# Kernel tuning notes

Hardware: AMD Instinct MI355X
Metric: run time of the kernel (lower is better)

Reference implementation:

```python
import jax, jax.numpy as jnp
import numpy as np

B, S, D, H, FC, O = 256, 512, 512, 512, 64, 2
E_CONST = 2.7183  # constant used in map_elapse_time


def setup_inputs() -> dict:
    key = jax.random.key(0)
    ks = jax.random.split(key, 24)
    std = 0.1
    w = lambda k, a, b: jax.random.normal(k, (a, b), jnp.float32) * std
    return {
        "x": jax.random.normal(ks[0], (B, S, D), jnp.float32),
        "time": jax.random.uniform(ks[1], (B, S), jnp.float32) * 10.0,  # positive elapsed times
        "Wi": w(ks[2], D, H), "Ui": w(ks[3], H, H), "bi": jnp.ones((H,), jnp.float32),
        "Wf": w(ks[4], D, H), "Uf": w(ks[5], H, H), "bf": jnp.ones((H,), jnp.float32),
        "Wog": w(ks[6], D, H), "Uog": w(ks[7], H, H), "bog": jnp.ones((H,), jnp.float32),
        "Wc": w(ks[8], D, H), "Uc": w(ks[9], H, H), "bc": jnp.ones((H,), jnp.float32),
        "W_decomp": w(ks[10], H, H), "b_decomp": jnp.ones((H,), jnp.float32),
        "Wo": w(ks[11], H, FC), "bo": jnp.ones((FC,), jnp.float32),
        "W_softmax": w(ks[12], FC, O), "b_softmax": jnp.ones((O,), jnp.float32),
    }


def reference(x, time, Wi, Ui, bi, Wf, Uf, bf, Wog, Uog, bog, Wc, Uc, bc,
              W_decomp, b_decomp, Wo, bo, W_softmax, b_softmax):
    Bsz, _, _ = x.shape
    Hd = Ui.shape[0]
    xs = jnp.swapaxes(x, 0, 1)                     # [S, B, D]
    ts = jnp.swapaxes(time, 0, 1)[..., None]       # [S, B, 1]
    h0 = jnp.zeros((Bsz, Hd), x.dtype)

    def step(carry, inp):
        h, c = carry
        x_t, t_t = inp
        # time-decay cell decomposition
        T = 1.0 / jnp.log(t_t + E_CONST)           # [B, 1] broadcast over H
        C_ST = jnp.tanh(c @ W_decomp + b_decomp)
        c = c - C_ST + T * C_ST
        # gates
        i = jax.nn.sigmoid(x_t @ Wi + h @ Ui + bi)
        f = jax.nn.sigmoid(x_t @ Wf + h @ Uf + bf)
        o = jax.nn.sigmoid(x_t @ Wog + h @ Uog + bog)
        Cn = jnp.tanh(x_t @ Wc + h @ Uc + bc)
        c = f * c + i * Cn
        h = o * jnp.tanh(c)
        return (h, c), None

    (h_last, _), _ = jax.lax.scan(step, (h0, h0), (xs, ts))
    # output head on last hidden state (dropout omitted: inference reference)
    fc = jax.nn.relu(h_last @ Wo + bo)
    return fc @ W_softmax + b_softmax             # [B, output_dim]
```

## Files before the change

### kernel.cpp

```cpp
#include <hip/hip_runtime.h>


typedef _Float16 f16;
typedef _Float16 f16x8 __attribute__((ext_vector_type(8)));
typedef float f32x4 __attribute__((ext_vector_type(4)));

#define B_ 256
#define S_ 512
#define D_ 512
#define H_ 512

#define WS_WTG  0u
#define WS_WTD  4194304u
#define WS_H16  4718592u
#define WS_C16  5242880u
#define WS_HF32 5767168u
#define WS_BAR  6291456u
#define WS_END  6295552u

__device__ __forceinline__ float fast_sigmoid(float x) {
  return 1.0f / (1.0f + __expf(-x));
}
__device__ __forceinline__ float fast_tanh(float x) {
  x = fminf(15.0f, fmaxf(-15.0f, x));
  float e = __expf(2.0f * x);
  return (e - 1.0f) / (e + 1.0f);
}
__device__ __forceinline__ unsigned pack_f16x2(float a, float b) {
  union { f16 h[2]; unsigned u; } p;
  p.h[0] = (f16)a; p.h[1] = (f16)b;
  return p.u;
}
__device__ __forceinline__ unsigned ld_agent(const unsigned* p) {
  return __hip_atomic_load(p, __ATOMIC_RELAXED, __HIP_MEMORY_SCOPE_AGENT);
}
__device__ __forceinline__ void st_agent(unsigned* p, unsigned v) {
  __hip_atomic_store(p, v, __ATOMIC_RELAXED, __HIP_MEMORY_SCOPE_AGENT);
}

__global__ void pack_weights(const float* __restrict__ Wi, const float* __restrict__ Ui,
                             const float* __restrict__ Wf, const float* __restrict__ Uf,
                             const float* __restrict__ Wog, const float* __restrict__ Uog,
                             const float* __restrict__ Wc, const float* __restrict__ Uc,
                             const float* __restrict__ Wd,
                             f16* __restrict__ wtg, f16* __restrict__ wtd)
{
  const int idx = blockIdx.x * 256 + threadIdx.x;
  if (idx < 2048 * 1024) {
    const int n = idx >> 10, k = idx & 1023;
    const int g = n >> 9, j = n & 511;
    const float* W[8] = {Wi, Ui, Wf, Uf, Wog, Uog, Wc, Uc};
    const float* src = W[(g << 1) + (k >> 9)];
    wtg[idx] = (f16)src[(size_t)(k & 511) * 512 + j];
  } else {
    const int i2 = idx - 2048 * 1024;
    const int n = i2 >> 9, k = i2 & 511;
    wtd[i2] = (f16)Wd[(size_t)k * 512 + n];
  }
}

__global__ void __launch_bounds__(256, 1)
tlstm_main(const float* __restrict__ x, const float* __restrict__ tim,
           const float* __restrict__ bi, const float* __restrict__ bf,
           const float* __restrict__ bog, const float* __restrict__ bc,
           const float* __restrict__ bdec,
           const f16* __restrict__ wtg, const f16* __restrict__ wtd,
           f16* __restrict__ h16, f16* __restrict__ c16,
           float* __restrict__ hf32, int* __restrict__ bar)
{
  __shared__ __align__(16) f16 Ag[16][1032];
  __shared__ __align__(16) f16 Ad[16][520];
  __shared__ float accS[10][272];
  __shared__ float biasS[10][16];

  const int tid  = threadIdx.x;
  const int lane = tid & 63;
  const int wv   = tid >> 6;
  const int l15  = lane & 15;
  const int lq   = lane >> 4;
  const int bid  = blockIdx.x;
  const int rowg = bid & 15;
  const int colg = bid >> 4;
  const int row0 = rowg << 4;
  const int jc0  = colg << 5;

  f16x8 Bg[4][2][8];
  #pragma unroll
  for (int g = 0; g < 4; ++g)
    #pragma unroll
    for (int ct = 0; ct < 2; ++ct) {
      const int n = (g << 9) + jc0 + (ct << 4) + l15;
      #pragma unroll
      for (int t = 0; t < 8; ++t) {
        const int k = ((wv << 3) + t) * 32 + (lq << 3);
        Bg[g][ct][t] = *(const f16x8*)(wtg + (size_t)n * 1024 + k);
      }
    }
  f16x8 Bd[2][4];
  #pragma unroll
  for (int ct = 0; ct < 2; ++ct) {
    const int n = jc0 + (ct << 4) + l15;
    #pragma unroll
    for (int t = 0; t < 4; ++t) {
      const int k = ((wv << 2) + t) * 32 + (lq << 3);
      Bd[ct][t] = *(const f16x8*)(wtd + (size_t)n * 512 + k);
    }
  }

  if (tid < 160) {
    const int u = tid >> 4, c = tid & 15;
    const float* bp = (u < 2) ? bi : (u < 4) ? bf : (u < 6) ? bog : (u < 8) ? bc : bdec;
    biasS[u][c] = bp[jc0 + ((u & 1) << 4) + c];
  }
  __syncthreads();

  const f16* AgF = &Ag[0][0];
  const f16* AdF = &Ad[0][0];
  const int a_base  = l15 * 1032 + (lq << 3);
  const int ad_base = l15 * 520 + (lq << 3);

  const int er   = tid >> 4;
  const int eq   = tid & 15;
  const int gb_e = row0 + er;
  float c_reg[2] = {0.f, 0.f};

  int* const my_bar = &bar[rowg * 64];

  for (int s = 0; s < S_; ++s) {
    const int cur = s & 1, nxt = cur ^ 1;
    const f16* hcur = h16 + (size_t)cur * (B_ * H_);
    const f16* ccur = c16 + (size_t)cur * (B_ * H_);

    {
      const int r = tid >> 4, c = tid & 15;
      const int li = r * 17 + c;
      #pragma unroll
      for (int u = 0; u < 10; ++u) accS[u][li] = biasS[u][c];
    }

    #pragma unroll
    for (int rr = 0; rr < 4; ++rr) {
      const int r = (wv << 2) + rr;
      const int gb = row0 + r;
      const float4* xr = (const float4*)(x + ((size_t)gb * S_ + s) * D_);
      float4 v0 = xr[lane * 2];
      float4 v1 = xr[lane * 2 + 1];
      f16x8 xv;
      xv[0] = (f16)v0.x; xv[1] = (f16)v0.y; xv[2] = (f16)v0.z; xv[3] = (f16)v0.w;
      xv[4] = (f16)v1.x; xv[5] = (f16)v1.y; xv[6] = (f16)v1.z; xv[7] = (f16)v1.w;
      *(f16x8*)&Ag[r][lane << 3] = xv;
      const unsigned* hp = (const unsigned*)(hcur + (size_t)gb * H_) + (lane << 2);
      const unsigned* cp = (const unsigned*)(ccur + (size_t)gb * H_) + (lane << 2);
      uint4 hv4, cv4;
      hv4.x = ld_agent(hp + 0); hv4.y = ld_agent(hp + 1);
      hv4.z = ld_agent(hp + 2); hv4.w = ld_agent(hp + 3);
      cv4.x = ld_agent(cp + 0); cv4.y = ld_agent(cp + 1);
      cv4.z = ld_agent(cp + 2); cv4.w = ld_agent(cp + 3);
      *(uint4*)&Ag[r][512 + (lane << 3)] = hv4;
      *(uint4*)&Ad[r][lane << 3]         = cv4;
    }
    __syncthreads();

    f32x4 acc[10];
    #pragma unroll
    for (int u = 0; u < 10; ++u) acc[u] = (f32x4){0.f, 0.f, 0.f, 0.f};
    #pragma unroll
    for (int t = 0; t < 8; ++t) {
      f16x8 a = *(const f16x8*)(AgF + a_base + ((wv << 3) + t) * 32);
      #pragma unroll
      for (int g = 0; g < 4; ++g)
        #pragma unroll
        for (int ct = 0; ct < 2; ++ct)
          acc[(g << 1) + ct] =
              __builtin_amdgcn_mfma_f32_16x16x32_f16(a, Bg[g][ct][t], acc[(g << 1) + ct], 0, 0, 0);
    }
    #pragma unroll
    for (int t = 0; t < 4; ++t) {
      f16x8 a = *(const f16x8*)(AdF + ad_base + ((wv << 2) + t) * 32);
      acc[8] = __builtin_amdgcn_mfma_f32_16x16x32_f16(a, Bd[0][t], acc[8], 0, 0, 0);
      acc[9] = __builtin_amdgcn_mfma_f32_16x16x32_f16(a, Bd[1][t], acc[9], 0, 0, 0);
    }
    #pragma unroll
    for (int u = 0; u < 10; ++u)
      #pragma unroll
      for (int i = 0; i < 4; ++i)
        atomicAdd(&accS[u][((lq << 2) + i) * 17 + l15], acc[u][i]);
    __syncthreads();

    {
      const float tv = tim[(size_t)gb_e * S_ + s];
      const float T  = 1.0f / __logf(tv + 2.7183f);
      float hv[2];
      #pragma unroll
      for (int j = 0; j < 2; ++j) {
        const int cc = (eq << 1) + j;
        const int ct = cc >> 4, cl = cc & 15;
        const int li = er * 17 + cl;
        const float pi = accS[0 + ct][li];
        const float pf = accS[2 + ct][li];
        const float po = accS[4 + ct][li];
        const float pc = accS[6 + ct][li];
        const float ps = accS[8 + ct][li];
        const float cst  = fast_tanh(ps);
        const float chat = c_reg[j] - cst + T * cst;
        const float cnew = fast_sigmoid(pf) * chat + fast_sigmoid(pi) * fast_tanh(pc);
        const float hnew = fast_sigmoid(po) * fast_tanh(cnew);
        c_reg[j] = cnew;
        hv[j] = hnew;
      }
      const size_t off = (size_t)gb_e * H_ + jc0 + (eq << 1);
      st_agent((unsigned*)(h16 + (size_t)nxt * (B_ * H_) + off), pack_f16x2(hv[0], hv[1]));
      st_agent((unsigned*)(c16 + (size_t)nxt * (B_ * H_) + off), pack_f16x2(c_reg[0], c_reg[1]));
      if (s == S_ - 1) {
        *(float2*)(hf32 + off) = make_float2(hv[0], hv[1]);
      }
    }
    __syncthreads();

    if (s != S_ - 1) {
      if (tid == 0) {
        asm volatile("s_waitcnt vmcnt(0)" ::: "memory");
        __hip_atomic_fetch_add(my_bar, 1, __ATOMIC_RELAXED, __HIP_MEMORY_SCOPE_AGENT);
        while (__hip_atomic_load(my_bar, __ATOMIC_RELAXED, __HIP_MEMORY_SCOPE_AGENT)
               < 16 * (s + 1))
          __builtin_amdgcn_s_sleep(1);
      }
      __syncthreads();
    }
  }
}

__global__ void head_kernel(const float* __restrict__ hf32,
                            const float* __restrict__ Wo, const float* __restrict__ bo,
                            const float* __restrict__ Wsm, const float* __restrict__ bsm,
                            float* __restrict__ out)
{
  __shared__ float fcS[4][64];
  const int tid = threadIdx.x;
  const int r = tid >> 6, j = tid & 63;
  const int b = blockIdx.x * 4 + r;
  const float* h = hf32 + (size_t)b * 512;
  float acc = 0.f;
  #pragma unroll 8
  for (int k = 0; k < 512; ++k) acc += h[k] * Wo[k * 64 + j];
  fcS[r][j] = fmaxf(acc + bo[j], 0.f);
  __syncthreads();
  if (tid < 8) {
    const int rr = tid >> 1, o = tid & 1;
    float s = bsm[o];
    #pragma unroll 8
    for (int jj = 0; jj < 64; ++jj) s += fcS[rr][jj] * Wsm[jj * 2 + o];
    out[(size_t)(blockIdx.x * 4 + rr) * 2 + o] = s;
  }
}

extern "C" void kernel_launch(void* const* d_in, const int* in_sizes, int n_in,
                              void* d_out, int out_size, void* d_ws, size_t ws_size,
                              hipStream_t stream)
{
  if (ws_size < (size_t)WS_END) return;

  const float* x    = (const float*)d_in[0];
  const float* tim  = (const float*)d_in[1];
  const float* Wi   = (const float*)d_in[2];
  const float* Ui   = (const float*)d_in[3];
  const float* bi   = (const float*)d_in[4];
  const float* Wf   = (const float*)d_in[5];
  const float* Uf   = (const float*)d_in[6];
  const float* bf   = (const float*)d_in[7];
  const float* Wog  = (const float*)d_in[8];
  const float* Uog  = (const float*)d_in[9];
  const float* bog  = (const float*)d_in[10];
  const float* Wc   = (const float*)d_in[11];
  const float* Uc   = (const float*)d_in[12];
  const float* bc   = (const float*)d_in[13];
  const float* Wd   = (const float*)d_in[14];
  const float* bd   = (const float*)d_in[15];
  const float* Wo   = (const float*)d_in[16];
  const float* bo   = (const float*)d_in[17];
  const float* Wsm  = (const float*)d_in[18];
  const float* bsm  = (const float*)d_in[19];

  char* ws    = (char*)d_ws;
  f16*  wtg   = (f16*)(ws + WS_WTG);
  f16*  wtd   = (f16*)(ws + WS_WTD);
  f16*  h16   = (f16*)(ws + WS_H16);
  f16*  c16   = (f16*)(ws + WS_C16);
  float* hf32 = (float*)(ws + WS_HF32);
  int*  bar   = (int*)(ws + WS_BAR);

  (void)hipMemsetAsync(ws + WS_H16, 0, WS_END - WS_H16, stream);

  pack_weights<<<9216, 256, 0, stream>>>(Wi, Ui, Wf, Uf, Wog, Uog, Wc, Uc, Wd, wtg, wtd);
  tlstm_main<<<256, 256, 0, stream>>>(x, tim, bi, bf, bog, bc, bd, wtg, wtd,
                                      h16, c16, hf32, bar);
  head_kernel<<<64, 256, 0, stream>>>(hf32, Wo, bo, Wsm, bsm, (float*)d_out);
}
```

Measured before the change: 10.32 ms.

## Split grid barrier into arrive/wait and overlap x loads with wait

The per-step grid barrier is split: the arrive increment moves to the top of the next step and the spin-wait happens after the x-tile loads and bias initialisation, so that independent work overlaps barrier latency. The scalar agent-scope atomic loads of h and c are replaced with inline-asm vectorised dwordx4 loads using the sc1 cache bit, issued after the wait. The arrive no longer waits on vmcnt(0) explicitly, so correctness relies on the preceding __syncthreads and sc1 coherence for the h/c stores being visible to other blocks.

New measurement: 9.325 ms. 1.11x faster.

```diff
diff --git a/kernel.cpp b/kernel.cpp
--- a/kernel.cpp
+++ b/kernel.cpp
@@ -4,6 +4,7 @@
 typedef _Float16 f16;
 typedef _Float16 f16x8 __attribute__((ext_vector_type(8)));
 typedef float f32x4 __attribute__((ext_vector_type(4)));
+typedef unsigned u32x4 __attribute__((ext_vector_type(4)));
 
 #define B_ 256
 #define S_ 512
@@ -30,9 +31,6 @@
   union { f16 h[2]; unsigned u; } p;
   p.h[0] = (f16)a; p.h[1] = (f16)b;
   return p.u;
-}
-__device__ __forceinline__ unsigned ld_agent(const unsigned* p) {
-  return __hip_atomic_load(p, __ATOMIC_RELAXED, __HIP_MEMORY_SCOPE_AGENT);
 }
 __device__ __forceinline__ void st_agent(unsigned* p, unsigned v) {
   __hip_atomic_store(p, v, __ATOMIC_RELAXED, __HIP_MEMORY_SCOPE_AGENT);
@@ -125,18 +123,15 @@
   float c_reg[2] = {0.f, 0.f};
 
   int* const my_bar = &bar[rowg * 64];
+  const int gb0 = row0 + (wv << 2);
 
   for (int s = 0; s < S_; ++s) {
     const int cur = s & 1, nxt = cur ^ 1;
     const f16* hcur = h16 + (size_t)cur * (B_ * H_);
     const f16* ccur = c16 + (size_t)cur * (B_ * H_);
 
-    {
-      const int r = tid >> 4, c = tid & 15;
-      const int li = r * 17 + c;
-      #pragma unroll
-      for (int u = 0; u < 10; ++u) accS[u][li] = biasS[u][c];
-    }
+    if (s > 0 && tid == 0)
+      __hip_atomic_fetch_add(my_bar, 1, __ATOMIC_RELAXED, __HIP_MEMORY_SCOPE_AGENT);
 
     #pragma unroll
     for (int rr = 0; rr < 4; ++rr) {
@@ -149,15 +144,48 @@
       xv[0] = (f16)v0.x; xv[1] = (f16)v0.y; xv[2] = (f16)v0.z; xv[3] = (f16)v0.w;
       xv[4] = (f16)v1.x; xv[5] = (f16)v1.y; xv[6] = (f16)v1.z; xv[7] = (f16)v1.w;
       *(f16x8*)&Ag[r][lane << 3] = xv;
-      const unsigned* hp = (const unsigned*)(hcur + (size_t)gb * H_) + (lane << 2);
-      const unsigned* cp = (const unsigned*)(ccur + (size_t)gb * H_) + (lane << 2);
-      uint4 hv4, cv4;
-      hv4.x = ld_agent(hp + 0); hv4.y = ld_agent(hp + 1);
-      hv4.z = ld_agent(hp + 2); hv4.w = ld_agent(hp + 3);
-      cv4.x = ld_agent(cp + 0); cv4.y = ld_agent(cp + 1);
-      cv4.z = ld_agent(cp + 2); cv4.w = ld_agent(cp + 3);
-      *(uint4*)&Ag[r][512 + (lane << 3)] = hv4;
-      *(uint4*)&Ad[r][lane << 3]         = cv4;
+    }
+    {
+      const int r = tid >> 4, c = tid & 15;
+      const int li = r * 17 + c;
+      #pragma unroll
+      for (int u = 0; u < 10; ++u) accS[u][li] = biasS[u][c];
+    }
+
+    if (s > 0 && tid == 0) {
+      while (__hip_atomic_load(my_bar, __ATOMIC_RELAXED, __HIP_MEMORY_SCOPE_AGENT)
+             < 16 * s)
+        __builtin_amdgcn_s_sleep(1);
+    }
+    __syncthreads();
+
+    {
+      const f16* hp = hcur + (size_t)gb0 * H_ + (lane << 3);
+      const f16* cp = ccur + (size_t)gb0 * H_ + (lane << 3);
+      u32x4 h0, h1, h2, h3, c0, c1, c2, c3;
+      asm volatile(
+        "global_load_dwordx4 %0, %8, off sc1\n\t"
+        "global_load_dwordx4 %1, %8, off offset:1024 sc1\n\t"
+        "global_load_dwordx4 %2, %8, off offset:2048 sc1\n\t"
+        "global_load_dwordx4 %3, %8, off offset:3072 sc1\n\t"
+        "global_load_dwordx4 %4, %9, off sc1\n\t"
+        "global_load_dwordx4 %5, %9, off offset:1024 sc1\n\t"
+        "global_load_dwordx4 %6, %9, off offset:2048 sc1\n\t"
+        "global_load_dwordx4 %7, %9, off offset:3072 sc1\n\t"
+        "s_waitcnt vmcnt(0)"
+        : "=&v"(h0), "=&v"(h1), "=&v"(h2), "=&v"(h3),
+          "=&v"(c0), "=&v"(c1), "=&v"(c2), "=&v"(c3)
+        : "v"(hp), "v"(cp)
+        : "memory");
+      const int r = wv << 2;
+      *(u32x4*)&Ag[r + 0][512 + (lane << 3)] = h0;
+      *(u32x4*)&Ag[r + 1][512 + (lane << 3)] = h1;
+      *(u32x4*)&Ag[r + 2][512 + (lane << 3)] = h2;
+      *(u32x4*)&Ag[r + 3][512 + (lane << 3)] = h3;
+      *(u32x4*)&Ad[r + 0][lane << 3] = c0;
+      *(u32x4*)&Ad[r + 1][lane << 3] = c1;
+      *(u32x4*)&Ad[r + 2][lane << 3] = c2;
+      *(u32x4*)&Ad[r + 3][lane << 3] = c3;
     }
     __syncthreads();
 
@@ -216,17 +244,6 @@
       }
     }
     __syncthreads();
-
-    if (s != S_ - 1) {
-      if (tid == 0) {
-        asm volatile("s_waitcnt vmcnt(0)" ::: "memory");
-        __hip_atomic_fetch_add(my_bar, 1, __ATOMIC_RELAXED, __HIP_MEMORY_SCOPE_AGENT);
-        while (__hip_atomic_load(my_bar, __ATOMIC_RELAXED, __HIP_MEMORY_SCOPE_AGENT)
-               < 16 * (s + 1))
-          __builtin_amdgcn_s_sleep(1);
-      }
-      __syncthreads();
-    }
   }
 }
 
```
